# Optimization experiments

Hardware: AMD Instinct MI355X
Metric: run time of the kernel (lower is better)

Reference implementation:

```python
import jax, jax.numpy as jnp
import numpy as np

H = 10          # heads
DIMS = [4, 256, 256, 256, 256, 256, 256, 2]  # model_param
B = 32768
OBS_X, OBS_Y, R = 0.0, 7.0, 4.0
L1, L2 = 3.0, 3.0


def _linear_params(key, din, dout, n=H):
    kw, kb = jax.random.split(key)
    s = 1.0 / np.sqrt(din)
    W = jax.random.uniform(kw, (n, dout, din), jnp.float32, -s, s)
    b = jax.random.uniform(kb, (n, dout), jnp.float32, -s, s)
    return W, b


def setup_inputs() -> dict:
    key = jax.random.key(0)
    ks = jax.random.split(key, 16)
    inp = {
        "x": jax.random.normal(ks[0], (B, DIMS[0]), jnp.float32),
        "sgn": 1,
        "wt": jnp.ones((H,), jnp.float32),
        "mean": jnp.zeros((DIMS[0],), jnp.float32),
        "std": jnp.ones((DIMS[0],), jnp.float32),
        "mean_label": jnp.zeros((DIMS[7],), jnp.float32),
        "std_label": jnp.ones((DIMS[7],), jnp.float32),
    }
    inp["W1"], inp["b1"] = _linear_params(ks[1], DIMS[0], DIMS[1])
    inp["W2"], inp["b2"] = _linear_params(ks[2], DIMS[1], DIMS[2])
    inp["W31"], inp["b31"] = _linear_params(ks[3], DIMS[2], DIMS[3])
    inp["W32"], inp["b32"] = _linear_params(ks[4], DIMS[2], DIMS[4])
    inp["W41"], inp["b41"] = _linear_params(ks[5], DIMS[3], DIMS[5])
    inp["W42"], inp["b42"] = _linear_params(ks[6], DIMS[4], DIMS[6])
    inp["W51"], inp["b51"] = _linear_params(ks[7], DIMS[5], DIMS[7])
    inp["W52"], inp["b52"] = _linear_params(ks[8], DIMS[6], DIMS[7])
    return inp


def _forward(x, W1, b1, W2, b2, W31, b31, W32, b32, W41, b41, W42, b42,
             W51, b51, W52, b52, wt, mean, std, mean_label, std_label):
    relu = jax.nn.relu
    x0 = x * std + mean                                   # de-normalized state [B,4]

    # Stacked per-head MLP (heads axis h)
    x1 = relu(jnp.einsum('bi,hoi->hbo', x, W1) + b1[:, None, :])
    x2 = relu(jnp.einsum('hbi,hoi->hbo', x1, W2) + b2[:, None, :])
    x31 = relu(jnp.einsum('hbi,hoi->hbo', x2, W31) + b31[:, None, :])
    x32 = relu(jnp.einsum('hbi,hoi->hbo', x2, W32) + b32[:, None, :])
    x41 = relu(jnp.einsum('hbi,hoi->hbo', x31, W41) + b41[:, None, :])
    x42 = relu(jnp.einsum('hbi,hoi->hbo', x32, W42) + b42[:, None, :])
    x51 = jnp.einsum('hbi,hoi->hbo', x41, W51) + b51[:, None, :]       # [H,B,2] QP linear cost
    x52 = 4.0 * jax.nn.sigmoid(jnp.einsum('hbi,hoi->hbo', x42, W52) + b52[:, None, :])  # [H,B,2] CBF gains

    # CBF geometric quantities (shared across heads)
    t1, w1, t2, w2 = x0[:, 0], x0[:, 1], x0[:, 2], x0[:, 3]
    s1, s2, c1, c2 = jnp.sin(t1), jnp.sin(t2), jnp.cos(t1), jnp.cos(t2)
    px = L1 * c1 + L2 * c2 - OBS_X
    py = L1 * s1 + L2 * s2 - OBS_Y
    vx = -L1 * s1 * w1 - L2 * s2 * w2
    vy = L1 * c1 * w1 + L2 * c2 * w2
    barrier = px ** 2 + py ** 2 - R ** 2
    b_dot = 2 * px * vx + 2 * py * vy
    Lf2b = (2 * vx ** 2 + 2 * vy ** 2
            + 2 * px * (-L1 * c1 * w1 ** 2 - L2 * c2 * w2 ** 2)
            + 2 * py * (-L1 * s1 * w1 ** 2 - L2 * s2 * w2 ** 2))
    LgLfbu1 = 2 * px * (-L1 * s1) + 2 * py * (L1 * c1)
    LgLfbu2 = 2 * px * (-L2 * s2) + 2 * py * (L2 * c2)
    g = jnp.stack([-LgLfbu1, -LgLfbu2], axis=-1)          # [B,2] constraint row

    # h uses head-0's x52[:,0] for every head (self.x52 caching in the torch code)
    a0 = x52[0, :, 0]                                     # [B]
    b_i = x52[:, :, 1]                                    # [H,B]
    h = Lf2b[None] + (a0[None] + b_i) * b_dot[None] + a0[None] * b_i * barrier[None]  # [H,B]

    # QP min 0.5 u'u + p'u  s.t. g.u <= h  -> closed-form halfspace projection
    u_unc = -x51                                          # [H,B,2]
    gg = jnp.sum(g * g, axis=-1)                          # [B]
    viol = jnp.einsum('hbc,bc->hb', u_unc, g) - h         # [H,B]
    lam = jnp.maximum(viol, 0.0) / gg[None]               # active-set multiplier
    u = u_unc - lam[..., None] * g[None]                  # [H,B,2]
    u = (u - mean_label) / std_label

    w = jax.nn.softmax(wt)                                # exp(wt)/sum(exp(wt))
    return jnp.einsum('h,hbc->bc', w, u)                  # [B,2]


def reference(x, sgn, wt, mean, std, mean_label, std_label,
              W1, b1, W2, b2, W31, b31, W32, b32, W41, b41, W42, b42,
              W51, b51, W52, b52):
    return _forward(x, W1, b1, W2, b2, W31, b31, W32, b32, W41, b41,
                    W42, b42, W51, b51, W52, b52, wt, mean, std,
                    mean_label, std_label)
```

## Files before the change

### kernel.cpp

```cpp
#include <hip/hip_runtime.h>
#include <hip/hip_bf16.h>

typedef __attribute__((ext_vector_type(8)))  short bf16x8_t;
typedef __attribute__((ext_vector_type(16))) float f32x16_t;
typedef __attribute__((ext_vector_type(4)))  float f32x4_t;

#define HN 10
#define BN 32768
#define DH 256
#define MT 64

#define KS17 17
#define HE17   (KS17*8*64*8)
#define ARRE17 (HN*HE17)

#define OFF_ABUF  0
#define OFF_S5    32768
#define SMEM_BYTES 33280

#define MFMA32 __builtin_amdgcn_mfma_f32_32x32x16_bf16

__device__ __forceinline__ unsigned swzoff(int row, int colb) {
  return (unsigned)(row * 512 + (colb ^ ((row & 31) << 4)));
}

__device__ __forceinline__ unsigned short f2bf(float v) {
  __hip_bfloat16 hb = __float2bfloat16(v);
  return *reinterpret_cast<unsigned short*>(&hb);
}
__device__ __forceinline__ unsigned pk2bf(float lo, float hi_) {
  return (unsigned)f2bf(lo) | ((unsigned)f2bf(hi_) << 16);
}

struct WPtrs { const float* w[5]; const float* b[5]; };

extern "C" __global__ void pack_big(WPtrs p, unsigned short* __restrict__ dst)
{
  int g = blockIdx.x * blockDim.x + threadIdx.x;
  if (g >= 5 * HN * KS17 * 8 * 64) return;
  int lane = g & 63; int t = g >> 6;
  int nt = t & 7; t >>= 3;
  int ks = t % KS17; t /= KS17;
  int h = t % HN;
  int a = t / HN;
  int col = nt * 32 + (lane & 31);
  int hi = lane >> 5;
  unsigned short* d = dst + (size_t)a * ARRE17 + (size_t)h * HE17
                    + ((ks * 8 + nt) * 64 + lane) * 8;
  if (ks < 16) {
    const float* src = p.w[a] + (size_t)h * 65536 + col * 256 + ks * 16 + hi * 8;
    #pragma unroll
    for (int j = 0; j < 8; ++j) d[j] = f2bf(src[j]);
  } else {
    float bv = p.b[a][(size_t)h * 256 + col];
    #pragma unroll
    for (int j = 0; j < 8; ++j) d[j] = (hi == 0 && j == 0) ? f2bf(bv) : (unsigned short)0;
  }
}

extern "C" __global__ void pack_w5(const float* __restrict__ w51, const float* __restrict__ w52,
                                   const float* __restrict__ b51, const float* __restrict__ b52,
                                   unsigned short* __restrict__ dst)
{
  int g = blockIdx.x * blockDim.x + threadIdx.x;
  if (g >= 2 * HN * KS17 * 64) return;
  int lane = g & 63; int t = g >> 6;
  int ks = t % KS17; t /= KS17;
  int h = t % HN;
  int br = t / HN;
  const float* w = br ? w52 : w51;
  const float* b = br ? b52 : b51;
  int col = lane & 31;
  int hi = lane >> 5;
  unsigned short* d = dst + ((size_t)(br * HN + h) * KS17 + ks) * 512 + lane * 8;
  if (ks < 16) {
    int k = ks * 16 + hi * 8;
    #pragma unroll
    for (int j = 0; j < 8; ++j) {
      float v = (col < 2) ? w[(size_t)h * 512 + col * 256 + k + j] : 0.f;
      d[j] = f2bf(v);
    }
  } else {
    float bv = (col < 2) ? b[(size_t)h * 2 + col] : 0.f;
    #pragma unroll
    for (int j = 0; j < 8; ++j) d[j] = (hi == 0 && j == 0) ? f2bf(bv) : (unsigned short)0;
  }
}

extern "C" __global__ void pack_w1(const float* __restrict__ w1, const float* __restrict__ b1,
                                   unsigned short* __restrict__ dst)
{
  int g = blockIdx.x * blockDim.x + threadIdx.x;
  if (g >= HN * 8 * 64) return;
  int lane = g & 63; int t = g >> 6;
  int nt = t & 7;
  int h = t >> 3;
  int col = nt * 32 + (lane & 31);
  int hi = lane >> 5;
  unsigned short* d = dst + (size_t)h * 4096 + ((size_t)nt * 64 + lane) * 8;
  #pragma unroll
  for (int j = 0; j < 8; ++j) {
    int k = hi * 8 + j;
    float v = 0.f;
    if (k < 4)       v = w1[(size_t)h * 1024 + col * 4 + k];
    else if (k == 4) v = b1[(size_t)h * 256 + col];
    d[j] = f2bf(v);
  }
}


__device__ __forceinline__ void write_actT(char* abuf, const f32x16_t acc[2][2],
                                           int lane, int wave)
{
  const int r31 = lane & 31, hi = lane >> 5;
  #pragma unroll
  for (int mt = 0; mt < 2; ++mt) {
    const int row = mt * 32 + r31;
    #pragma unroll
    for (int nt = 0; nt < 2; ++nt) {
      #pragma unroll
      for (int g = 0; g < 4; ++g) {
        const int col0 = (wave * 2 + nt) * 32 + 8 * g + 4 * hi;
        unsigned w0 = pk2bf(fmaxf(acc[mt][nt][4 * g + 0], 0.f),
                            fmaxf(acc[mt][nt][4 * g + 1], 0.f));
        unsigned w1 = pk2bf(fmaxf(acc[mt][nt][4 * g + 2], 0.f),
                            fmaxf(acc[mt][nt][4 * g + 3], 0.f));
        unsigned long long pk = (unsigned long long)w0 | ((unsigned long long)w1 << 32);
        *(unsigned long long*)(abuf + swzoff(row, col0 * 2)) = pk;
      }
    }
  }
}

__device__ __forceinline__ void gemm_ip(char* abuf,
                                        const unsigned short* __restrict__ wl,
                                        int lane, int wave, bf16x8_t ones)
{
  const int r31 = lane & 31, hi = lane >> 5;
  f32x16_t acc[2][2];
  #pragma unroll
  for (int mt = 0; mt < 2; ++mt)
    #pragma unroll
    for (int nt = 0; nt < 2; ++nt)
      #pragma unroll
      for (int i = 0; i < 16; ++i) acc[mt][nt][i] = 0.f;

  const char* wb = (const char*)wl + (size_t)(wave * 2) * 1024 + (size_t)lane * 16;
  bf16x8_t c0[2], c1[2], c2[2];
  #pragma unroll
  for (int nt = 0; nt < 2; ++nt) {
    c0[nt] = *(const bf16x8_t*)(wb + nt * 1024);
    c1[nt] = *(const bf16x8_t*)(wb + 8192 + nt * 1024);
  }
  #pragma unroll
  for (int ks = 0; ks < KS17; ++ks) {
    if (ks < KS17 - 2) {
      #pragma unroll
      for (int nt = 0; nt < 2; ++nt)
        c2[nt] = *(const bf16x8_t*)(wb + (ks + 2) * 8192 + nt * 1024);
    }
    bf16x8_t a[2];
    #pragma unroll
    for (int mt = 0; mt < 2; ++mt)
      a[mt] = (ks < 16)
        ? *(const bf16x8_t*)(abuf + swzoff(mt * 32 + r31, ks * 32 + hi * 16))
        : ones;
    #pragma unroll
    for (int mt = 0; mt < 2; ++mt) {
      acc[mt][0] = MFMA32(c0[0], a[mt], acc[mt][0], 0, 0, 0);
      acc[mt][1] = MFMA32(c0[1], a[mt], acc[mt][1], 0, 0, 0);
    }
    #pragma unroll
    for (int nt = 0; nt < 2; ++nt) { c0[nt] = c1[nt]; c1[nt] = c2[nt]; }
  }
  __syncthreads();
  write_actT(abuf, acc, lane, wave);
  __syncthreads();
}

extern "C" __global__ __launch_bounds__(256, 3)
void abnet_main(const float* __restrict__ x,
                const unsigned short* __restrict__ wpk,
                const unsigned short* __restrict__ w5pk,
                const unsigned short* __restrict__ w1pk,
                float* __restrict__ ws51, float* __restrict__ ws52)
{
  extern __shared__ char smem[];
  char*  abuf = smem + OFF_ABUF;
  float* s5   = (float*)(smem + OFF_S5);

  const int tid  = threadIdx.x;
  const int lane = tid & 63, wave = tid >> 6;
  const int L  = (blockIdx.x & 7) * 1280 + (blockIdx.x >> 3);
  const int rt = L & 511;
  const int hb = L >> 9;
  const int h  = hb >> 1, br = hb & 1;
  const int row0 = rt * MT;

  const int r31 = lane & 31, hi = lane >> 5;

  bf16x8_t ones;
  #pragma unroll
  for (int j = 0; j < 8; ++j) ones[j] = 0;
  if (hi == 0) ones[0] = (short)0x3F80;

  {
    const char* w1b = (const char*)(w1pk + (size_t)h * 4096)
                    + (size_t)(wave * 2) * 1024 + (size_t)lane * 16;
    bf16x8_t wf[2];
    #pragma unroll
    for (int nt = 0; nt < 2; ++nt) wf[nt] = *(const bf16x8_t*)(w1b + nt * 1024);
    f32x16_t acc[2][2];
    #pragma unroll
    for (int mt = 0; mt < 2; ++mt)
      #pragma unroll
      for (int nt = 0; nt < 2; ++nt)
        #pragma unroll
        for (int i = 0; i < 16; ++i) acc[mt][nt][i] = 0.f;
    #pragma unroll
    for (int mt = 0; mt < 2; ++mt) {
      int row = row0 + mt * 32 + r31;
      f32x4_t xv = *(const f32x4_t*)(x + (size_t)row * 4);
      bf16x8_t af;
      #pragma unroll
      for (int j = 0; j < 8; ++j) {
        short v = 0;
        if (hi == 0) {
          if (j < 4)       v = (short)f2bf(xv[j]);
          else if (j == 4) v = (short)0x3F80;
        }
        af[j] = v;
      }
      acc[mt][0] = MFMA32(wf[0], af, acc[mt][0], 0, 0, 0);
      acc[mt][1] = MFMA32(wf[1], af, acc[mt][1], 0, 0, 0);
    }
    write_actT(abuf, acc, lane, wave);
    __syncthreads();
  }

  gemm_ip(abuf, wpk + (size_t)h * HE17,                             lane, wave, ones);
  gemm_ip(abuf, wpk + (size_t)(1 + br) * ARRE17 + (size_t)h * HE17, lane, wave, ones);
  gemm_ip(abuf, wpk + (size_t)(3 + br) * ARRE17 + (size_t)h * HE17, lane, wave, ones);

  if (wave < 2) {
    const unsigned short* w5 = w5pk + (size_t)(br * HN + h) * (KS17 * 512);
    const int mt = wave;
    f32x16_t acc;
    #pragma unroll
    for (int i = 0; i < 16; ++i) acc[i] = 0.f;
    #pragma unroll
    for (int ks = 0; ks < KS17; ++ks) {
      bf16x8_t a = (ks < 16)
        ? *(const bf16x8_t*)(abuf + swzoff(mt * 32 + r31, ks * 32 + hi * 16))
        : ones;
      bf16x8_t b = *(const bf16x8_t*)(w5 + (size_t)(ks * 64 + lane) * 8);
      acc = MFMA32(a, b, acc, 0, 0, 0);
    }
    if (r31 < 2) {
      #pragma unroll
      for (int r = 0; r < 16; ++r) {
        int row = mt * 32 + (r & 3) + 8 * (r >> 2) + 4 * hi;
        s5[row * 2 + r31] = acc[r];
      }
    }
  }
  __syncthreads();

  if (tid < 128) {
    int row = tid >> 1, c = tid & 1;
    float* wsout = br ? ws52 : ws51;
    wsout[((size_t)h * BN + row0 + row) * 2 + c] = s5[row * 2 + c];
  }
}

extern "C" __global__ __launch_bounds__(256)
void abnet_epi(const float* __restrict__ x, const float* __restrict__ wt,
               const float* __restrict__ mean, const float* __restrict__ stdv,
               const float* __restrict__ mlab, const float* __restrict__ slab,
               const float* __restrict__ ws51, const float* __restrict__ ws52,
               float* __restrict__ out)
{
  const int row = blockIdx.x * 256 + threadIdx.x;
  f32x4_t xr = *(const f32x4_t*)(x + (size_t)row * 4);
  float t1  = xr[0] * stdv[0] + mean[0];
  float w1v = xr[1] * stdv[1] + mean[1];
  float t2  = xr[2] * stdv[2] + mean[2];
  float w2v = xr[3] * stdv[3] + mean[3];
  float s1, c1, s2, c2;
  sincosf(t1, &s1, &c1);
  sincosf(t2, &s2, &c2);
  float px = 3.f * c1 + 3.f * c2;
  float py = 3.f * s1 + 3.f * s2 - 7.f;
  float vx = -3.f * s1 * w1v - 3.f * s2 * w2v;
  float vy =  3.f * c1 * w1v + 3.f * c2 * w2v;
  float e_bar  = px * px + py * py - 16.f;
  float e_bdot = 2.f * (px * vx + py * vy);
  float e_lf2b = 2.f * vx * vx + 2.f * vy * vy
               + 2.f * px * (-3.f * c1 * w1v * w1v - 3.f * c2 * w2v * w2v)
               + 2.f * py * (-3.f * s1 * w1v * w1v - 3.f * s2 * w2v * w2v);
  float e_g1 = 6.f * (px * s1 - py * c1);
  float e_g2 = 6.f * (px * s2 - py * c2);
  float e_ggi = 1.f / (e_g1 * e_g1 + e_g2 * e_g2);

  float m = wt[0];
  for (int i = 1; i < HN; ++i) m = fmaxf(m, wt[i]);
  float s = 0.f;
  for (int i = 0; i < HN; ++i) s += __expf(wt[i] - m);
  float sm_inv = 1.f / s;
  float ml0 = mlab[0], ml1 = mlab[1];
  float isl0 = 1.f / slab[0], isl1 = 1.f / slab[1];

  float a0r = 4.f / (1.f + __expf(-ws52[(size_t)row * 2 + 0]));
  float accu0 = 0.f, accu1 = 0.f;
  for (int h = 0; h < HN; ++h) {
    float u1 = -ws51[((size_t)h * BN + row) * 2 + 0];
    float u2 = -ws51[((size_t)h * BN + row) * 2 + 1];
    float bi = 4.f / (1.f + __expf(-ws52[((size_t)h * BN + row) * 2 + 1]));
    float hv   = e_lf2b + (a0r + bi) * e_bdot + a0r * bi * e_bar;
    float viol = u1 * e_g1 + u2 * e_g2 - hv;
    float lam  = fmaxf(viol, 0.f) * e_ggi;
    float uu1 = u1 - lam * e_g1;
    float uu2 = u2 - lam * e_g2;
    float whv = __expf(wt[h] - m) * sm_inv;
    accu0 += whv * (uu1 - ml0) * isl0;
    accu1 += whv * (uu2 - ml1) * isl1;
  }
  float2 o; o.x = accu0; o.y = accu1;
  *(float2*)(out + (size_t)row * 2) = o;
}

extern "C" void kernel_launch(void* const* d_in, const int* in_sizes, int n_in,
                              void* d_out, int out_size, void* d_ws, size_t ws_size,
                              hipStream_t stream)
{
  const float* x    = (const float*)d_in[0];
  const float* wt   = (const float*)d_in[2];
  const float* mean = (const float*)d_in[3];
  const float* stdv = (const float*)d_in[4];
  const float* mlab = (const float*)d_in[5];
  const float* slab = (const float*)d_in[6];
  const float* W1   = (const float*)d_in[7];
  const float* b1   = (const float*)d_in[8];
  WPtrs wp;
  wp.w[0] = (const float*)d_in[9];
  wp.w[1] = (const float*)d_in[11];
  wp.w[2] = (const float*)d_in[13];
  wp.w[3] = (const float*)d_in[15];
  wp.w[4] = (const float*)d_in[17];
  wp.b[0] = (const float*)d_in[10];
  wp.b[1] = (const float*)d_in[12];
  wp.b[2] = (const float*)d_in[14];
  wp.b[3] = (const float*)d_in[16];
  wp.b[4] = (const float*)d_in[18];
  const float* W51 = (const float*)d_in[19];
  const float* b51 = (const float*)d_in[20];
  const float* W52 = (const float*)d_in[21];
  const float* b52 = (const float*)d_in[22];

  char* wsb = (char*)d_ws;
  unsigned short* wpk  = (unsigned short*)wsb;
  unsigned short* w5pk = (unsigned short*)(wsb + 6963200);
  unsigned short* w1pk = (unsigned short*)(wsb + 7311360);
  float* ws51 = (float*)(wsb + 7393280);
  float* ws52 = (float*)(wsb + 10014720);

  hipLaunchKernelGGL(pack_big, dim3(1700), dim3(256), 0, stream, wp, wpk);
  hipLaunchKernelGGL(pack_w5,  dim3(85),   dim3(256), 0, stream, W51, W52, b51, b52, w5pk);
  hipLaunchKernelGGL(pack_w1,  dim3(20),   dim3(256), 0, stream, W1, b1, w1pk);

  (void)hipFuncSetAttribute(reinterpret_cast<const void*>(abnet_main),
                            hipFuncAttributeMaxDynamicSharedMemorySize, SMEM_BYTES);
  hipLaunchKernelGGL(abnet_main, dim3(512 * HN * 2), dim3(256), SMEM_BYTES, stream,
                     x, wpk, w5pk, w1pk, ws51, ws52);
  hipLaunchKernelGGL(abnet_epi, dim3(BN / 256), dim3(256), 0, stream,
                     x, wt, mean, stdv, mlab, slab, ws51, ws52, (float*)d_out);
}
```

Measured before the change: 291.5 us.

## Compute shared trunk once per block and run both branches with ping-pong buffers

Each block now processes both branches for its head and row tile instead of one, so layer 1 and layer 2 are computed once rather than twice. A second shared-memory activation buffer keeps the layer-2 output alive while each branch runs in place on the other buffer. This halves the grid and doubles shared memory per block, lowering the occupancy target from 3 to 2 blocks per CU.

```diff
diff --git a/kernel.cpp b/kernel.cpp
--- a/kernel.cpp
+++ b/kernel.cpp
@@ -14,9 +14,10 @@
 #define HE17   (KS17*8*64*8)
 #define ARRE17 (HN*HE17)
 
-#define OFF_ABUF  0
-#define OFF_S5    32768
-#define SMEM_BYTES 33280
+#define OFF_A     0
+#define OFF_B     32768
+#define OFF_S5    65536
+#define SMEM_BYTES 66560
 
 #define MFMA32 __builtin_amdgcn_mfma_f32_32x32x16_bf16
 
@@ -109,7 +110,7 @@
 }
 
 
-__device__ __forceinline__ void write_actT(char* abuf, const f32x16_t acc[2][2],
+__device__ __forceinline__ void write_actT(char* sout, const f32x16_t acc[2][2],
                                            int lane, int wave)
 {
   const int r31 = lane & 31, hi = lane >> 5;
@@ -126,13 +127,14 @@
         unsigned w1 = pk2bf(fmaxf(acc[mt][nt][4 * g + 2], 0.f),
                             fmaxf(acc[mt][nt][4 * g + 3], 0.f));
         unsigned long long pk = (unsigned long long)w0 | ((unsigned long long)w1 << 32);
-        *(unsigned long long*)(abuf + swzoff(row, col0 * 2)) = pk;
+        *(unsigned long long*)(sout + swzoff(row, col0 * 2)) = pk;
       }
     }
   }
 }
 
-__device__ __forceinline__ void gemm_ip(char* abuf,
+template<bool INPLACE>
+__device__ __forceinline__ void gemm_pp(const char* sin, char* sout,
                                         const unsigned short* __restrict__ wl,
                                         int lane, int wave, bf16x8_t ones)
 {
@@ -163,7 +165,7 @@
     #pragma unroll
     for (int mt = 0; mt < 2; ++mt)
       a[mt] = (ks < 16)
-        ? *(const bf16x8_t*)(abuf + swzoff(mt * 32 + r31, ks * 32 + hi * 16))
+        ? *(const bf16x8_t*)(sin + swzoff(mt * 32 + r31, ks * 32 + hi * 16))
         : ones;
     #pragma unroll
     for (int mt = 0; mt < 2; ++mt) {
@@ -173,12 +175,47 @@
     #pragma unroll
     for (int nt = 0; nt < 2; ++nt) { c0[nt] = c1[nt]; c1[nt] = c2[nt]; }
   }
+  if (INPLACE) __syncthreads();
+  write_actT(sout, acc, lane, wave);
   __syncthreads();
-  write_actT(abuf, acc, lane, wave);
+}
+
+__device__ __forceinline__ void final_pp(const char* sin, float* s5,
+                                         const unsigned short* __restrict__ w5,
+                                         float* __restrict__ wsout,
+                                         int row0, int tid, int lane, int wave,
+                                         bf16x8_t ones)
+{
+  const int r31 = lane & 31, hi = lane >> 5;
+  if (wave < 2) {
+    const int mt = wave;
+    f32x16_t acc;
+    #pragma unroll
+    for (int i = 0; i < 16; ++i) acc[i] = 0.f;
+    #pragma unroll
+    for (int ks = 0; ks < KS17; ++ks) {
+      bf16x8_t a = (ks < 16)
+        ? *(const bf16x8_t*)(sin + swzoff(mt * 32 + r31, ks * 32 + hi * 16))
+        : ones;
+      bf16x8_t b = *(const bf16x8_t*)(w5 + (size_t)(ks * 64 + lane) * 8);
+      acc = MFMA32(a, b, acc, 0, 0, 0);
+    }
+    if (r31 < 2) {
+      #pragma unroll
+      for (int r = 0; r < 16; ++r) {
+        int row = mt * 32 + (r & 3) + 8 * (r >> 2) + 4 * hi;
+        s5[row * 2 + r31] = acc[r];
+      }
+    }
+  }
   __syncthreads();
-}
-
-extern "C" __global__ __launch_bounds__(256, 3)
+  if (tid < 128) {
+    int row = tid >> 1, c = tid & 1;
+    wsout[(size_t)(row0 + row) * 2 + c] = s5[row * 2 + c];
+  }
+}
+
+extern "C" __global__ __launch_bounds__(256, 2)
 void abnet_main(const float* __restrict__ x,
                 const unsigned short* __restrict__ wpk,
                 const unsigned short* __restrict__ w5pk,
@@ -186,15 +223,15 @@
                 float* __restrict__ ws51, float* __restrict__ ws52)
 {
   extern __shared__ char smem[];
-  char*  abuf = smem + OFF_ABUF;
+  char*  bufA = smem + OFF_A;
+  char*  bufB = smem + OFF_B;
   float* s5   = (float*)(smem + OFF_S5);
 
   const int tid  = threadIdx.x;
   const int lane = tid & 63, wave = tid >> 6;
-  const int L  = (blockIdx.x & 7) * 1280 + (blockIdx.x >> 3);
+  const int L  = (blockIdx.x & 7) * 640 + (blockIdx.x >> 3);
   const int rt = L & 511;
-  const int hb = L >> 9;
-  const int h  = hb >> 1, br = hb & 1;
+  const int h  = L >> 9;
   const int row0 = rt * MT;
 
   const int r31 = lane & 31, hi = lane >> 5;
@@ -234,43 +271,27 @@
       acc[mt][0] = MFMA32(wf[0], af, acc[mt][0], 0, 0, 0);
       acc[mt][1] = MFMA32(wf[1], af, acc[mt][1], 0, 0, 0);
     }
-    write_actT(abuf, acc, lane, wave);
+    write_actT(bufA, acc, lane, wave);
     __syncthreads();
   }
 
-  gemm_ip(abuf, wpk + (size_t)h * HE17,                             lane, wave, ones);
-  gemm_ip(abuf, wpk + (size_t)(1 + br) * ARRE17 + (size_t)h * HE17, lane, wave, ones);
-  gemm_ip(abuf, wpk + (size_t)(3 + br) * ARRE17 + (size_t)h * HE17, lane, wave, ones);
-
-  if (wave < 2) {
-    const unsigned short* w5 = w5pk + (size_t)(br * HN + h) * (KS17 * 512);
-    const int mt = wave;
-    f32x16_t acc;
-    #pragma unroll
-    for (int i = 0; i < 16; ++i) acc[i] = 0.f;
-    #pragma unroll
-    for (int ks = 0; ks < KS17; ++ks) {
-      bf16x8_t a = (ks < 16)
-        ? *(const bf16x8_t*)(abuf + swzoff(mt * 32 + r31, ks * 32 + hi * 16))
-        : ones;
-      bf16x8_t b = *(const bf16x8_t*)(w5 + (size_t)(ks * 64 + lane) * 8);
-      acc = MFMA32(a, b, acc, 0, 0, 0);
-    }
-    if (r31 < 2) {
-      #pragma unroll
-      for (int r = 0; r < 16; ++r) {
-        int row = mt * 32 + (r & 3) + 8 * (r >> 2) + 4 * hi;
-        s5[row * 2 + r31] = acc[r];
-      }
-    }
-  }
-  __syncthreads();
-
-  if (tid < 128) {
-    int row = tid >> 1, c = tid & 1;
-    float* wsout = br ? ws52 : ws51;
-    wsout[((size_t)h * BN + row0 + row) * 2 + c] = s5[row * 2 + c];
-  }
+  const unsigned short* W2  = wpk + (size_t)h * HE17;
+  const unsigned short* W31 = wpk + 1 * (size_t)ARRE17 + (size_t)h * HE17;
+  const unsigned short* W32 = wpk + 2 * (size_t)ARRE17 + (size_t)h * HE17;
+  const unsigned short* W41 = wpk + 3 * (size_t)ARRE17 + (size_t)h * HE17;
+  const unsigned short* W42 = wpk + 4 * (size_t)ARRE17 + (size_t)h * HE17;
+
+  gemm_pp<false>(bufA, bufB, W2, lane, wave, ones);
+
+  gemm_pp<false>(bufB, bufA, W31, lane, wave, ones);
+  gemm_pp<true >(bufA, bufA, W41, lane, wave, ones);
+  final_pp(bufA, s5, w5pk + (size_t)h * (KS17 * 512),
+           ws51 + (size_t)h * BN * 2, row0, tid, lane, wave, ones);
+
+  gemm_pp<false>(bufB, bufA, W32, lane, wave, ones);
+  gemm_pp<true >(bufA, bufA, W42, lane, wave, ones);
+  final_pp(bufA, s5, w5pk + (size_t)(HN + h) * (KS17 * 512),
+           ws52 + (size_t)h * BN * 2, row0, tid, lane, wave, ones);
 }
 
 extern "C" __global__ __launch_bounds__(256)
@@ -370,7 +391,7 @@
 
   (void)hipFuncSetAttribute(reinterpret_cast<const void*>(abnet_main),
                             hipFuncAttributeMaxDynamicSharedMemorySize, SMEM_BYTES);
-  hipLaunchKernelGGL(abnet_main, dim3(512 * HN * 2), dim3(256), SMEM_BYTES, stream,
+  hipLaunchKernelGGL(abnet_main, dim3(512 * HN), dim3(256), SMEM_BYTES, stream,
                      x, wpk, w5pk, w1pk, ws51, ws52);
   hipLaunchKernelGGL(abnet_epi, dim3(BN / 256), dim3(256), 0, stream,
                      x, wt, mean, stdv, mlab, slab, ws51, ws52, (float*)d_out);
```

Measured after the change: 263.9 us. 1.1x faster.
